# Performance work log

Measured on AMD Instinct MI355X. Metric: run time of the kernel, lower is better.

Reference implementation:

```python
import jax, jax.numpy as jnp
import numpy as np
import math

B, N, DQ, DK, DV, H = 8, 1024, 512, 512, 512, 8


def setup_inputs() -> dict:
    key = jax.random.key(0)
    ks = jax.random.split(key, 9)
    s = 0.02
    return {
        "Q": jax.random.normal(ks[0], (B, N, DQ), jnp.float32),
        "K": jax.random.normal(ks[1], (B, N, DK), jnp.float32),
        "mask": jax.random.bernoulli(ks[2], 0.9, (B, N)).astype(jnp.float32),
        "Wq": jax.random.normal(ks[3], (DQ, DV), jnp.float32) * s,
        "bq": jnp.zeros((DV,), jnp.float32),
        "Wk": jax.random.normal(ks[4], (DK, DV), jnp.float32) * s,
        "bk": jnp.zeros((DV,), jnp.float32),
        "Wv": jax.random.normal(ks[5], (DK, DV), jnp.float32) * s,
        "bv": jnp.zeros((DV,), jnp.float32),
        "Wo": jax.random.normal(ks[6], (DV, DV), jnp.float32) * s,
        "bo": jnp.zeros((DV,), jnp.float32),
    }


def reference(Q, K, mask, Wq, bq, Wk, bk, Wv, bv, Wo, bo):
    b, n, _ = Q.shape
    dV = Wq.shape[1]
    dh = dV // H
    scale = 1.0 / math.sqrt(dV)
    m = mask[..., None]                      # [B,N,1]
    Qp = (Q @ Wq + bq) * m                   # [B,N,dV]
    Kp = (K @ Wk + bk) * m
    Vp = (K @ Wv + bv) * m
    # torch.cat(x.split(dh,2),0) == head-major stacking -> keep as [H,B,N,dh]
    q = Qp.reshape(b, n, H, dh).transpose(2, 0, 1, 3)
    k = Kp.reshape(b, n, H, dh).transpose(2, 0, 1, 3)
    v = Vp.reshape(b, n, H, dh).transpose(2, 0, 1, 3)
    S = jnp.einsum('hbnd,hbmd->hbnm', q, k) * scale   # [H,B,N,N]
    mx = jnp.max(S, axis=3, keepdims=True)            # unmasked row max (faithful)
    m1 = mask[None, :, :, None]                       # [1,B,N,1]
    m2 = mask[None, :, None, :]                       # [1,B,1,N]
    num = jnp.exp((S - mx) * m1 * m2) * m1 * m2
    A = num / (jnp.sum(num, axis=3, keepdims=True) + 1e-16)
    O = q + jnp.einsum('hbnm,hbmd->hbnd', A, v)       # residual on Q_
    O = O.transpose(1, 2, 0, 3).reshape(b, n, dV)     # un-split heads
    O = O + jax.nn.relu((O @ Wo + bo) * m)
    return O
```

## Files before the change

### kernel.cpp

```cpp
#include <hip/hip_runtime.h>

typedef short bf16x8 __attribute__((ext_vector_type(8)));
typedef float f32x4 __attribute__((ext_vector_type(4)));
typedef float f32x16 __attribute__((ext_vector_type(16)));

#define MFMA16(a, b, c) __builtin_amdgcn_mfma_f32_16x16x32_bf16((a), (b), (c), 0, 0, 0)
#define MFMA32(a, b, c) __builtin_amdgcn_mfma_f32_32x32x16_bf16((a), (b), (c), 0, 0, 0)

#define GLOAD_LDS16(g, l)                                              \
  __builtin_amdgcn_global_load_lds(                                    \
      (const __attribute__((address_space(1))) unsigned int*)(g),      \
      (__attribute__((address_space(3))) unsigned int*)(l), 16, 0, 0)

__device__ __forceinline__ unsigned short f2b(float f) {
  union { float f; unsigned int u; } x; x.f = f;
  unsigned int r = x.u + 0x7FFFu + ((x.u >> 16) & 1u);
  return (unsigned short)(r >> 16);
}
__device__ __forceinline__ float b2f(unsigned short h) {
  union { unsigned int u; float f; } x; x.u = ((unsigned int)h) << 16;
  return x.f;
}
__device__ __forceinline__ unsigned int cvtpk(float lo, float hi) {
  unsigned int r;
  asm("v_cvt_pk_bf16_f32 %0, %1, %2" : "=v"(r) : "v"(lo), "v"(hi));
  return r;
}
__device__ __forceinline__ short cvt1(float x) {
  return (short)(unsigned short)cvtpk(x, x);
}
__device__ __forceinline__ float vexp2(float x) {
  float r;
  asm("v_exp_f32 %0, %1" : "=v"(r) : "v"(x));
  return r;
}

#define SCALE2 0.06375870724f

__global__ __launch_bounds__(256) void prep_kernel(
    const float* __restrict__ Wq, const float* __restrict__ Wk,
    const float* __restrict__ Wv, const float* __restrict__ Wo,
    const float* __restrict__ Q, const float* __restrict__ K,
    const float* __restrict__ mask,
    short* __restrict__ Wt, short* __restrict__ Qb, short* __restrict__ Kb,
    short* __restrict__ mbf) {
  __shared__ float tile[64][65];
  const int bid = blockIdx.x;
  const int t = threadIdx.x;
  if (bid < 256) {
    const int z = bid >> 6;
    const int rem = bid & 63;
    const int k0 = (rem >> 3) * 64, n0 = (rem & 7) * 64;
    const float* W = (z == 0) ? Wq : (z == 1) ? Wk : (z == 2) ? Wv : Wo;
    const float ws = (z == 1) ? SCALE2 : 1.0f;
    const int r = t >> 4, cc = (t & 15) * 4;
#pragma unroll
    for (int it = 0; it < 4; ++it) {
      int row = r + it * 16;
      const float4 v = *(const float4*)(W + (k0 + row) * 512 + n0 + cc);
      tile[row][cc + 0] = v.x; tile[row][cc + 1] = v.y;
      tile[row][cc + 2] = v.z; tile[row][cc + 3] = v.w;
    }
    __syncthreads();
    short* out = Wt + z * (512 * 512);
#pragma unroll
    for (int it = 0; it < 4; ++it) {
      int nrow = r + it * 16;
      unsigned int u0 = cvtpk(tile[cc + 0][nrow] * ws, tile[cc + 1][nrow] * ws);
      unsigned int u1 = cvtpk(tile[cc + 2][nrow] * ws, tile[cc + 3][nrow] * ws);
      uint2 uv; uv.x = u0; uv.y = u1;
      *(uint2*)(out + (n0 + nrow) * 512 + k0 + cc) = uv;
    }
  } else {
    const int idx = bid - 256;
    const int ybit = idx >> 11;
    const int x = idx & 2047;
    if (ybit == 0 && x < 4) {
      int i = (x * 256 + t) * 8;
      float4 a = *(const float4*)(mask + i);
      float4 bb = *(const float4*)(mask + i + 4);
      unsigned int m0 = (a.x != 0.f) ? 0x3F80u : 0u;
      unsigned int m1 = (a.y != 0.f) ? 0x3F80u : 0u;
      unsigned int m2 = (a.z != 0.f) ? 0x3F80u : 0u;
      unsigned int m3 = (a.w != 0.f) ? 0x3F80u : 0u;
      unsigned int m4 = (bb.x != 0.f) ? 0x3F80u : 0u;
      unsigned int m5 = (bb.y != 0.f) ? 0x3F80u : 0u;
      unsigned int m6 = (bb.z != 0.f) ? 0x3F80u : 0u;
      unsigned int m7 = (bb.w != 0.f) ? 0x3F80u : 0u;
      uint4 mm;
      mm.x = m0 | (m1 << 16); mm.y = m2 | (m3 << 16);
      mm.z = m4 | (m5 << 16); mm.w = m6 | (m7 << 16);
      *(uint4*)(mbf + i) = mm;
    }
    const float* src = ybit ? K : Q;
    short* dst = ybit ? Kb : Qb;
    int i = (x * 256 + t) * 8;
    float4 v0 = *(const float4*)(src + i);
    float4 v1 = *(const float4*)(src + i + 4);
    uint2 a, b;
    a.x = cvtpk(v0.x, v0.y); a.y = cvtpk(v0.z, v0.w);
    b.x = cvtpk(v1.x, v1.y); b.y = cvtpk(v1.z, v1.w);
    *(uint2*)(dst + i) = a;
    *(uint2*)(dst + i + 4) = b;
  }
}

__device__ __forceinline__ void gemm_bf16_core(
    const short* __restrict__ A, const short* __restrict__ Wt,
    short* Lb, int m0, int t, f32x4 acc[4][4]) {
  const int lane = t & 63, w = t >> 6;
  const int c = lane & 15, g = lane >> 4;
  const int wr = w >> 1, wc = w & 1;
  const int lr = lane >> 3;
  const int sswz = ((lane & 7) ^ lr) << 3;
  const int swc = (c & 7) << 3;
  short* Al = Lb;
  short* Bl = Lb + 8192;

  for (int kt = 0; kt < 8; ++kt) {
#pragma unroll
    for (int it = 0; it < 4; ++it) {
      int row = w * 32 + it * 8;
      GLOAD_LDS16(A + (size_t)(m0 + row + lr) * 512 + kt * 64 + sswz, Al + row * 64);
      GLOAD_LDS16(Wt + (size_t)(row + lr) * 512 + kt * 64 + sswz, Bl + row * 64);
    }
    __syncthreads();
    __builtin_amdgcn_s_setprio(1);
#pragma unroll
    for (int kc = 0; kc < 2; ++kc) {
      bf16x8 af[4], bfr[4];
#pragma unroll
      for (int mi = 0; mi < 4; ++mi) {
        int r = wr * 64 + mi * 16 + c;
        af[mi] = *(const bf16x8*)(Al + r * 64 + ((kc * 32 + 8 * g) ^ swc));
      }
#pragma unroll
      for (int ni = 0; ni < 4; ++ni) {
        int r = wc * 64 + ni * 16 + c;
        bfr[ni] = *(const bf16x8*)(Bl + r * 64 + ((kc * 32 + 8 * g) ^ swc));
      }
#pragma unroll
      for (int mi = 0; mi < 4; ++mi)
#pragma unroll
        for (int ni = 0; ni < 4; ++ni)
          acc[mi][ni] = MFMA16(af[mi], bfr[ni], acc[mi][ni]);
    }
    __builtin_amdgcn_s_setprio(0);
    __syncthreads();
  }
}

__global__ __launch_bounds__(256) void proj2_kernel(
    const short* __restrict__ Qb, const short* __restrict__ Kb,
    const short* __restrict__ Wt4,
    const float* __restrict__ bq, const float* __restrict__ bk, const float* __restrict__ bv,
    const float* __restrict__ maskf,
    short* __restrict__ Qp, short* __restrict__ Kp, short* __restrict__ Vt) {
  __shared__ short Lbuf[16384];
  const int by = blockIdx.y;
  const int m0 = blockIdx.x * 128;
  const int t = threadIdx.x;
  const short* A;
  const short* Wt;
  const float* bias;
  int nbase;
  if (by < 4) { A = Qb; nbase = by * 128; Wt = Wt4 + nbase * 512; bias = bq; }
  else if (by < 8) { A = Kb; nbase = (by - 4) * 128; Wt = Wt4 + 262144 + nbase * 512; bias = bk; }
  else { A = Kb; nbase = (by - 8) * 128; Wt = Wt4 + 524288 + nbase * 512; bias = bv; }
  const float bscale = (by >= 4 && by < 8) ? SCALE2 : 1.0f;

  const f32x4 zz = {0.f, 0.f, 0.f, 0.f};
  f32x4 acc[4][4];
#pragma unroll
  for (int mi = 0; mi < 4; ++mi)
#pragma unroll
    for (int ni = 0; ni < 4; ++ni) acc[mi][ni] = zz;
  gemm_bf16_core(A, Wt, Lbuf, m0, t, acc);

  const int lane = t & 63, w = t >> 6;
  const int c = lane & 15, g = lane >> 4;
  const int wr = w >> 1, wc = w & 1;
  float mk[4][4];
#pragma unroll
  for (int mi = 0; mi < 4; ++mi) {
    int mbase = m0 + wr * 64 + mi * 16 + 4 * g;
#pragma unroll
    for (int i = 0; i < 4; ++i) mk[mi][i] = maskf[mbase + i];
  }
  float bval[4];
#pragma unroll
  for (int ni = 0; ni < 4; ++ni) bval[ni] = bias[nbase + wc * 64 + ni * 16 + c] * bscale;

  if (by < 8) {
#pragma unroll
    for (int ni = 0; ni < 4; ++ni) {
      int nloc = wc * 64 + ni * 16 + c;
#pragma unroll
      for (int mi = 0; mi < 4; ++mi) {
#pragma unroll
        for (int i = 0; i < 4; ++i) {
          int mloc = wr * 64 + mi * 16 + 4 * g + i;
          float v = (acc[mi][ni][i] + bval[ni]) * mk[mi][i];
          Lbuf[mloc * 128 + (nloc ^ ((mloc & 7) << 3))] = cvt1(v);
        }
      }
    }
    __syncthreads();
    short* outp = (by < 4) ? Qp : Kp;
    const int rrow = t >> 4, rcol = (t & 15) * 8;
#pragma unroll
    for (int p = 0; p < 8; ++p) {
      int m = p * 16 + rrow;
      bf16x8 vv = *(const bf16x8*)(Lbuf + m * 128 + (rcol ^ ((m & 7) << 3)));
      *(bf16x8*)(outp + (size_t)(m0 + m) * 512 + nbase + rcol) = vv;
    }
  } else {
#pragma unroll
    for (int ni = 0; ni < 4; ++ni) {
      int nloc = wc * 64 + ni * 16 + c;
#pragma unroll
      for (int mi = 0; mi < 4; ++mi) {
        int mloc4 = wr * 64 + mi * 16 + 4 * g;
        unsigned int lo = cvtpk((acc[mi][ni][0] + bval[ni]) * mk[mi][0],
                                (acc[mi][ni][1] + bval[ni]) * mk[mi][1]);
        unsigned int hi = cvtpk((acc[mi][ni][2] + bval[ni]) * mk[mi][2],
                                (acc[mi][ni][3] + bval[ni]) * mk[mi][3]);
        int ma = (mloc4 & 15) + (((mloc4 >> 4) ^ (nloc & 7)) << 4);
        uint2 uv; uv.x = lo; uv.y = hi;
        *(uint2*)(Lbuf + nloc * 128 + ma) = uv;
      }
    }
    __syncthreads();
    const int rrow = t >> 4, rcol = (t & 15) * 8;
#pragma unroll
    for (int p = 0; p < 8; ++p) {
      int n = p * 16 + rrow;
      int ma = (rcol & 8) + (((rcol >> 4) ^ (n & 7)) << 4);
      bf16x8 vv = *(const bf16x8*)(Lbuf + n * 128 + ma);
      int d = nbase + n;
      int hh = d >> 6, dd = d & 63;
      int mg = m0 + rcol;
      int bi = mg >> 10, seq0 = mg & 1023;
      *(bf16x8*)(Vt + ((size_t)((bi * 8 + hh) * 64 + dd)) * 1024 + seq0) = vv;
    }
  }
}

__global__ __launch_bounds__(128, 3) void attn7_kernel(
    const short* __restrict__ Qp, const short* __restrict__ Kp,
    const short* __restrict__ Vt, const float* __restrict__ mask,
    const short* __restrict__ mbf, short* __restrict__ Obb) {
  __shared__ short Kl[2][32 * 128];
  __shared__ short Vl[2][32 * 128];
  __shared__ short Ml[1024];
  const int t = threadIdx.x, lane = t & 63, w = t >> 6;
  const int q32 = lane & 31, hi = lane >> 5;
  const int hw = blockIdx.x;
  const int L = (hw & 7) * 128 + (hw >> 3);
  const int qt = L & 15, head = L >> 4;
  const int b = head & 7, h = head >> 3;
  const int n0 = qt * 64 + w * 32;

  const short* Kg = Kp + (size_t)(b * 1024) * 512 + h * 64;
  const short* Vg = Vt + (size_t)((b * 8 + h) * 64) * 1024;

  bf16x8 qf[4];
  {
    const short* qptr = Qp + ((size_t)(b * 1024 + n0 + q32) * 512 + h * 64 + 8 * hi);
#pragma unroll
    for (int kk = 0; kk < 4; ++kk) qf[kk] = *(const bf16x8*)(qptr + 16 * kk);
  }
  asm volatile("s_waitcnt vmcnt(0)" ::: "memory");
  __builtin_amdgcn_sched_barrier(0);

  auto STAGE = [&](int kvt, int buf) {
    const int kr = kvt * 64;
    short* Kd = &Kl[buf][0];
    short* Vd = &Vl[buf][0];
#pragma unroll
    for (int it = 0; it < 4; ++it) {
      int rb = it * 8 + w * 4;
      int r2 = rb + (lane >> 4);
      int sx = (lane & 15) ^ (r2 & 15);
      GLOAD_LDS16(Kg + (size_t)(kr + 2 * r2 + (sx >> 3)) * 512 + (sx & 7) * 8, Kd + rb * 128);
    }
#pragma unroll
    for (int it = 0; it < 4; ++it) {
      int rb = it * 8 + w * 4;
      int rv = rb + (lane >> 4);
      int sx = (lane & 15) ^ (rv & 15);
      GLOAD_LDS16(Vg + (size_t)(2 * rv + (sx >> 3)) * 1024 + kr + (sx & 7) * 8, Vd + rb * 128);
    }
  };

  GLOAD_LDS16(mbf + b * 1024 + w * 512 + lane * 8, Ml + w * 512);
  STAGE(0, 0);
  STAGE(1, 1);

  f32x16 o0, o1, suma;
#pragma unroll
  for (int e = 0; e < 16; ++e) { o0[e] = 0.f; o1[e] = 0.f; suma[e] = 0.f; }

#pragma unroll 1
  for (int kvt = 0; kvt < 16; ++kvt) {
    const int cur = kvt & 1;
    if (kvt < 15) { asm volatile("s_waitcnt vmcnt(8)" ::: "memory"); }
    else          { asm volatile("s_waitcnt vmcnt(0)" ::: "memory"); }
    __builtin_amdgcn_sched_barrier(0);
    __builtin_amdgcn_s_barrier();
    __builtin_amdgcn_sched_barrier(0);

#pragma unroll
    for (int half = 0; half < 2; ++half) {
      bf16x8 ka[4], va[2][2], mo[2];
      {
        const int kvr = 32 * half + q32;
        const int r2 = kvr >> 1;
#pragma unroll
        for (int kk = 0; kk < 4; ++kk) {
          int sx = ((((kvr & 1) << 3) | (2 * kk + hi)) ^ (r2 & 15));
          ka[kk] = *(const bf16x8*)(&Kl[cur][0] + r2 * 128 + sx * 8);
        }
      }
#pragma unroll
      for (int ds = 0; ds < 2; ++ds) {
        const int d = 32 * ds + q32;
        const int rv = d >> 1;
#pragma unroll
        for (int ch = 0; ch < 2; ++ch) {
          int sx = ((((d & 1) << 3) | (4 * half + 2 * ch + hi)) ^ (rv & 15));
          va[ds][ch] = *(const bf16x8*)(&Vl[cur][0] + rv * 128 + sx * 8);
        }
      }
#pragma unroll
      for (int ch = 0; ch < 2; ++ch)
        mo[ch] = *(const bf16x8*)(Ml + kvt * 64 + 32 * half + 16 * ch + 8 * hi);

      __builtin_amdgcn_sched_barrier(0);
      asm volatile("s_waitcnt lgkmcnt(0)" ::: "memory");
      __builtin_amdgcn_sched_barrier(0);
      if (half == 1) {
        __builtin_amdgcn_s_barrier();
        __builtin_amdgcn_sched_barrier(0);
        if (kvt < 14) STAGE(kvt + 2, cur);
        __builtin_amdgcn_sched_barrier(0);
      }

      f32x16 s0;
#pragma unroll
      for (int e = 0; e < 16; ++e) s0[e] = 0.f;
      __builtin_amdgcn_s_setprio(1);
#pragma unroll
      for (int kk = 0; kk < 4; ++kk) s0 = MFMA32(ka[kk], qf[kk], s0);
      __builtin_amdgcn_s_setprio(0);

      f32x16 p0;
#pragma unroll
      for (int e = 0; e < 16; ++e) p0[e] = vexp2(s0[e]);

      bf16x8 pf[2];
#pragma unroll
      for (int ch = 0; ch < 2; ++ch) {
        unsigned int w01a = cvtpk(p0[8 * ch + 0], p0[8 * ch + 1]);
        unsigned int w01b = cvtpk(p0[8 * ch + 2], p0[8 * ch + 3]);
        unsigned int w23a = cvtpk(p0[8 * ch + 4], p0[8 * ch + 5]);
        unsigned int w23b = cvtpk(p0[8 * ch + 6], p0[8 * ch + 7]);
        unsigned int x0 = hi ? w01a : w23a;
        unsigned int x1 = hi ? w01b : w23b;
        unsigned int g0 = (unsigned int)__shfl_xor((int)x0, 32);
        unsigned int g1 = (unsigned int)__shfl_xor((int)x1, 32);
        union { unsigned int u[4]; bf16x8 v; } pu;
        pu.u[0] = hi ? g0 : w01a;
        pu.u[1] = hi ? g1 : w01b;
        pu.u[2] = hi ? w23a : g0;
        pu.u[3] = hi ? w23b : g1;
        pf[ch] = pu.v;
      }

      __builtin_amdgcn_s_setprio(1);
#pragma unroll
      for (int ch = 0; ch < 2; ++ch) {
        o0 = MFMA32(va[0][ch], pf[ch], o0);
        o1 = MFMA32(va[1][ch], pf[ch], o1);
        suma = MFMA32(mo[ch], pf[ch], suma);
      }
      __builtin_amdgcn_s_setprio(0);
    }
  }

  short* Tw = &Kl[0][0] + w * 2304;
  const float inv = __builtin_amdgcn_rcpf(suma[0] + 1e-16f);
#pragma unroll
  for (int rr = 0; rr < 4; ++rr) {
    uint2 uv0, uv1;
    uv0.x = cvtpk(o0[4 * rr + 0] * inv, o0[4 * rr + 1] * inv);
    uv0.y = cvtpk(o0[4 * rr + 2] * inv, o0[4 * rr + 3] * inv);
    *(uint2*)(Tw + q32 * 68 + 8 * rr + 4 * hi) = uv0;
    uv1.x = cvtpk(o1[4 * rr + 0] * inv, o1[4 * rr + 1] * inv);
    uv1.y = cvtpk(o1[4 * rr + 2] * inv, o1[4 * rr + 3] * inv);
    *(uint2*)(Tw + q32 * 68 + 32 + 8 * rr + 4 * hi) = uv1;
  }
  asm volatile("s_waitcnt lgkmcnt(0)" ::: "memory");
  __builtin_amdgcn_sched_barrier(0);

  const int erow = lane >> 1, ecs = (lane & 1) * 8;
  const float mk1 = mask[b * 1024 + n0 + erow];
#pragma unroll
  for (int it = 0; it < 4; ++it) {
    int col = ecs + it * 16;
    bf16x8 av = *(const bf16x8*)(Tw + erow * 68 + col);
    const short* qptr = Qp + (size_t)(b * 1024 + n0 + erow) * 512 + h * 64 + col;
    bf16x8 qv = *(const bf16x8*)qptr;
    uint4 rr;
    rr.x = cvtpk(b2f((unsigned short)qv[0]) + mk1 * b2f((unsigned short)av[0]),
                 b2f((unsigned short)qv[1]) + mk1 * b2f((unsigned short)av[1]));
    rr.y = cvtpk(b2f((unsigned short)qv[2]) + mk1 * b2f((unsigned short)av[2]),
                 b2f((unsigned short)qv[3]) + mk1 * b2f((unsigned short)av[3]));
    rr.z = cvtpk(b2f((unsigned short)qv[4]) + mk1 * b2f((unsigned short)av[4]),
                 b2f((unsigned short)qv[5]) + mk1 * b2f((unsigned short)av[5]));
    rr.w = cvtpk(b2f((unsigned short)qv[6]) + mk1 * b2f((unsigned short)av[6]),
                 b2f((unsigned short)qv[7]) + mk1 * b2f((unsigned short)av[7]));
    *(uint4*)(Obb + (size_t)(b * 1024 + n0 + erow) * 512 + h * 64 + col) = rr;
  }
}

__global__ __launch_bounds__(256) void final2_kernel(
    const short* __restrict__ Obb,
    const short* __restrict__ Wto, const float* __restrict__ bo,
    const float* __restrict__ maskf, float* __restrict__ out) {
  __shared__ short Lbuf[16384];
  const int m0 = blockIdx.x * 128, n0 = blockIdx.y * 128;
  const int t = threadIdx.x;
  const f32x4 zz = {0.f, 0.f, 0.f, 0.f};
  f32x4 acc[4][4];
#pragma unroll
  for (int mi = 0; mi < 4; ++mi)
#pragma unroll
    for (int ni = 0; ni < 4; ++ni) acc[mi][ni] = zz;
  gemm_bf16_core(Obb, Wto + n0 * 512, Lbuf, m0, t, acc);

  const int lane = t & 63, w = t >> 6;
  const int c = lane & 15, g = lane >> 4;
  const int wr = w >> 1, wc = w & 1;
  float mk[4][4];
#pragma unroll
  for (int mi = 0; mi < 4; ++mi) {
    int mbase = m0 + wr * 64 + mi * 16 + 4 * g;
#pragma unroll
    for (int i = 0; i < 4; ++i) mk[mi][i] = maskf[mbase + i];
  }
#pragma unroll
  for (int ni = 0; ni < 4; ++ni) {
    int n = n0 + wc * 64 + ni * 16 + c;
    float bval = bo[n];
#pragma unroll
    for (int mi = 0; mi < 4; ++mi) {
      int mbase = m0 + wr * 64 + mi * 16 + 4 * g;
#pragma unroll
      for (int i = 0; i < 4; ++i) {
        float v = (acc[mi][ni][i] + bval) * mk[mi][i];
        v = fmaxf(v, 0.f);
        size_t off = (size_t)(mbase + i) * 512 + n;
        out[off] = b2f((unsigned short)Obb[off]) + v;
      }
    }
  }
}

extern "C" void kernel_launch(void* const* d_in, const int* in_sizes, int n_in,
                              void* d_out, int out_size, void* d_ws, size_t ws_size,
                              hipStream_t stream) {
  (void)in_sizes; (void)n_in; (void)out_size; (void)ws_size;
  const float* Q    = (const float*)d_in[0];
  const float* K    = (const float*)d_in[1];
  const float* mask = (const float*)d_in[2];
  const float* Wq   = (const float*)d_in[3];
  const float* bq   = (const float*)d_in[4];
  const float* Wk   = (const float*)d_in[5];
  const float* bk   = (const float*)d_in[6];
  const float* Wv   = (const float*)d_in[7];
  const float* bv   = (const float*)d_in[8];
  const float* Wo   = (const float*)d_in[9];
  const float* bo   = (const float*)d_in[10];

  char* ws = (char*)d_ws;
  const size_t MB = 1048576;
  short* Wt4 = (short*)ws;
  short* Qb  = (short*)(ws + 2 * MB);
  short* Kb  = (short*)(ws + 10 * MB);
  short* Qp  = (short*)(ws + 18 * MB);
  short* Kp  = (short*)(ws + 26 * MB);
  short* Vt  = (short*)(ws + 34 * MB);
  short* Obb = (short*)(ws + 42 * MB);
  short* mbf = (short*)(ws + 50 * MB);
  float* out = (float*)d_out;

  prep_kernel<<<dim3(4352), 256, 0, stream>>>(Wq, Wk, Wv, Wo, Q, K, mask, Wt4, Qb, Kb, mbf);
  proj2_kernel<<<dim3(64, 12), 256, 0, stream>>>(Qb, Kb, Wt4, bq, bk, bv, mask, Qp, Kp, Vt);
  attn7_kernel<<<dim3(1024), 128, 0, stream>>>(Qp, Kp, Vt, mask, mbf, Obb);
  final2_kernel<<<dim3(64, 4), 256, 0, stream>>>(Obb, Wt4 + 3 * 262144, bo, mask, out);
}
```

Before: 79.75 us.

## Single-buffer K/V tiles in attention kernel and raise occupancy hint to four

Replaces the double-buffered K/V shared-memory staging with a single buffer. The load of the next tile is issued mid-iteration, and each iteration waits for all outstanding loads. The launch-bounds minimum is raised from 3 to 4 blocks, so all 1024 blocks can be resident together on 256 CUs and the tail wave goes away. The cost is less prefetch overlap, since each tile must fully arrive before compute. A barrier is added before the epilogue reuses the K/V buffers as transpose scratch.

```diff
diff --git a/kernel.cpp b/kernel.cpp
--- a/kernel.cpp
+++ b/kernel.cpp
@@ -246,12 +246,12 @@
   }
 }
 
-__global__ __launch_bounds__(128, 3) void attn7_kernel(
+__global__ __launch_bounds__(128, 4) void attn10_kernel(
     const short* __restrict__ Qp, const short* __restrict__ Kp,
     const short* __restrict__ Vt, const float* __restrict__ mask,
     const short* __restrict__ mbf, short* __restrict__ Obb) {
-  __shared__ short Kl[2][32 * 128];
-  __shared__ short Vl[2][32 * 128];
+  __shared__ short Kl[32 * 128];
+  __shared__ short Vl[32 * 128];
   __shared__ short Ml[1024];
   const int t = threadIdx.x, lane = t & 63, w = t >> 6;
   const int q32 = lane & 31, hi = lane >> 5;
@@ -273,29 +273,26 @@
   asm volatile("s_waitcnt vmcnt(0)" ::: "memory");
   __builtin_amdgcn_sched_barrier(0);
 
-  auto STAGE = [&](int kvt, int buf) {
+  auto STAGE = [&](int kvt) {
     const int kr = kvt * 64;
-    short* Kd = &Kl[buf][0];
-    short* Vd = &Vl[buf][0];
 #pragma unroll
     for (int it = 0; it < 4; ++it) {
       int rb = it * 8 + w * 4;
       int r2 = rb + (lane >> 4);
       int sx = (lane & 15) ^ (r2 & 15);
-      GLOAD_LDS16(Kg + (size_t)(kr + 2 * r2 + (sx >> 3)) * 512 + (sx & 7) * 8, Kd + rb * 128);
+      GLOAD_LDS16(Kg + (size_t)(kr + 2 * r2 + (sx >> 3)) * 512 + (sx & 7) * 8, Kl + rb * 128);
     }
 #pragma unroll
     for (int it = 0; it < 4; ++it) {
       int rb = it * 8 + w * 4;
       int rv = rb + (lane >> 4);
       int sx = (lane & 15) ^ (rv & 15);
-      GLOAD_LDS16(Vg + (size_t)(2 * rv + (sx >> 3)) * 1024 + kr + (sx & 7) * 8, Vd + rb * 128);
+      GLOAD_LDS16(Vg + (size_t)(2 * rv + (sx >> 3)) * 1024 + kr + (sx & 7) * 8, Vl + rb * 128);
     }
   };
 
   GLOAD_LDS16(mbf + b * 1024 + w * 512 + lane * 8, Ml + w * 512);
-  STAGE(0, 0);
-  STAGE(1, 1);
+  STAGE(0);
 
   f32x16 o0, o1, suma;
 #pragma unroll
@@ -303,9 +300,7 @@
 
 #pragma unroll 1
   for (int kvt = 0; kvt < 16; ++kvt) {
-    const int cur = kvt & 1;
-    if (kvt < 15) { asm volatile("s_waitcnt vmcnt(8)" ::: "memory"); }
-    else          { asm volatile("s_waitcnt vmcnt(0)" ::: "memory"); }
+    asm volatile("s_waitcnt vmcnt(0)" ::: "memory");
     __builtin_amdgcn_sched_barrier(0);
     __builtin_amdgcn_s_barrier();
     __builtin_amdgcn_sched_barrier(0);
@@ -319,7 +314,7 @@
 #pragma unroll
         for (int kk = 0; kk < 4; ++kk) {
           int sx = ((((kvr & 1) << 3) | (2 * kk + hi)) ^ (r2 & 15));
-          ka[kk] = *(const bf16x8*)(&Kl[cur][0] + r2 * 128 + sx * 8);
+          ka[kk] = *(const bf16x8*)(Kl + r2 * 128 + sx * 8);
         }
       }
 #pragma unroll
@@ -329,7 +324,7 @@
 #pragma unroll
         for (int ch = 0; ch < 2; ++ch) {
           int sx = ((((d & 1) << 3) | (4 * half + 2 * ch + hi)) ^ (rv & 15));
-          va[ds][ch] = *(const bf16x8*)(&Vl[cur][0] + rv * 128 + sx * 8);
+          va[ds][ch] = *(const bf16x8*)(Vl + rv * 128 + sx * 8);
         }
       }
 #pragma unroll
@@ -342,7 +337,7 @@
       if (half == 1) {
         __builtin_amdgcn_s_barrier();
         __builtin_amdgcn_sched_barrier(0);
-        if (kvt < 14) STAGE(kvt + 2, cur);
+        if (kvt < 15) STAGE(kvt + 1);
         __builtin_amdgcn_sched_barrier(0);
       }
 
@@ -388,7 +383,9 @@
     }
   }
 
-  short* Tw = &Kl[0][0] + w * 2304;
+  __builtin_amdgcn_s_barrier();
+  __builtin_amdgcn_sched_barrier(0);
+  short* Tw = (w == 0) ? Kl : Vl;
   const float inv = __builtin_amdgcn_rcpf(suma[0] + 1e-16f);
 #pragma unroll
   for (int rr = 0; rr < 4; ++rr) {
@@ -497,6 +494,6 @@
 
   prep_kernel<<<dim3(4352), 256, 0, stream>>>(Wq, Wk, Wv, Wo, Q, K, mask, Wt4, Qb, Kb, mbf);
   proj2_kernel<<<dim3(64, 12), 256, 0, stream>>>(Qb, Kb, Wt4, bq, bk, bv, mask, Qp, Kp, Vt);
-  attn7_kernel<<<dim3(1024), 128, 0, stream>>>(Qp, Kp, Vt, mask, mbf, Obb);
+  attn10_kernel<<<dim3(1024), 128, 0, stream>>>(Qp, Kp, Vt, mask, mbf, Obb);
   final2_kernel<<<dim3(64, 4), 256, 0, stream>>>(Obb, Wt4 + 3 * 262144, bo, mask, out);
 }
```

New measurement: 136.4 us. 71.0% more time.
